# Kernel optimization log

Hardware: AMD Instinct MI355X
Metric: run time of the kernel (lower is better)

Reference implementation:

```python
import jax, jax.numpy as jnp
import numpy as np
from jax.scipy.special import logsumexp

K, V, D, R = 512, 50257, 768, 192
S_ITERS = 10
LAMBDA_MAHAL = 0.3
GAMMA_SINKHORN = 0.3


def setup_inputs() -> dict:
    key = jax.random.key(0)
    ks = jax.random.split(key, 6)
    word_embeds = jax.random.normal(ks[0], (V, D), dtype=jnp.float32)
    # warm-start anchors: mean word embed + small noise (as in torch init)
    anchors = jnp.broadcast_to(word_embeds.mean(axis=0, keepdims=True), (K, D)) \
        + jax.random.normal(ks[1], (K, D), dtype=jnp.float32) * 0.05
    return {
        "word_embeds": word_embeds,
        "concept_anchors": anchors,
        "M_U": jax.random.normal(ks[2], (D, R), dtype=jnp.float32) * 0.01,
        "log_eps": jnp.float32(-1.5),
        "log_scale": jnp.float32(0.0),
        "topic_bias": jnp.zeros((K, 1), dtype=jnp.float32),
        "word_proj_w": jnp.eye(D, dtype=jnp.float32),
    }


def _normalize(x, eps=1e-12):
    n = jnp.sqrt(jnp.sum(x * x, axis=-1, keepdims=True))
    return x / jnp.maximum(n, eps)


def _mahalanobis_cost(A, B, M_U):
    # M = I + U U^T  (low-rank update); C[k,v] = (a-b)^T M (a-b)
    M = jnp.eye(A.shape[-1], dtype=A.dtype) + M_U @ M_U.T
    MA = A @ M          # [K, D]
    MB = B @ M          # [V, D]
    AA = jnp.sum(MA * A, axis=-1, keepdims=True)       # [K, 1]
    BB = jnp.sum(MB * B, axis=-1, keepdims=True).T     # [1, V]
    AB = MA @ B.T                                      # [K, V]
    return jax.nn.relu(AA + BB - 2.0 * AB)


def _sinkhorn_log(log_K):
    def body(_, carry):
        log_u, log_v = carry
        log_u = -logsumexp(log_K + log_v, axis=1, keepdims=True)  # [K,1]
        log_v = -logsumexp(log_K + log_u, axis=0, keepdims=True)  # [1,V]
        return log_u, log_v
    log_u0 = jnp.zeros((log_K.shape[0], 1), log_K.dtype)
    log_v0 = jnp.zeros((1, log_K.shape[1]), log_K.dtype)
    log_u, log_v = jax.lax.fori_loop(0, S_ITERS, body, (log_u0, log_v0))
    return log_K + log_u + log_v


def reference(word_embeds, concept_anchors, M_U, log_eps, log_scale,
              topic_bias, word_proj_w):
    w = _normalize(word_embeds @ word_proj_w.T)     # [V, D]
    a = _normalize(concept_anchors)                 # [K, D]
    scale = jnp.minimum(jnp.exp(log_scale), 20.0)
    direct_logits = scale * (a @ w.T) + topic_bias  # [K, V]
    mahal = _mahalanobis_cost(a, w, M_U)            # [K, V]
    eps = jax.nn.softplus(log_eps) + 0.001
    log_P = _sinkhorn_log(-mahal / eps)             # [K, V]
    logits = direct_logits - LAMBDA_MAHAL * mahal + GAMMA_SINKHORN * log_P
    logits = jnp.clip(logits, -30.0, 30.0)
    return jax.nn.softmax(logits, axis=-1)
```

## Files before the change

### kernel.cpp

```cpp
#include <hip/hip_runtime.h>
#include <math.h>

#define KK 512
#define VV 50257
#define VP 50272
#define DD 768
#define RR 192

#define LAM 0.3f
#define GAM 0.3f
#define L2E 1.44269504088896340736f
#define ENC_NEG_INF 0x007FFFFFu

typedef __bf16 bf16x8 __attribute__((ext_vector_type(8)));
typedef _Float16 f16x8 __attribute__((ext_vector_type(8)));
typedef _Float16 f16x2 __attribute__((ext_vector_type(2)));
typedef unsigned short u16x8 __attribute__((ext_vector_type(8)));
typedef float f32x4 __attribute__((ext_vector_type(4)));

static __device__ __forceinline__ float get_eps(const float* p_log_eps) {
  return log1pf(expf(p_log_eps[0])) + 0.001f;
}

static __device__ __forceinline__ float fast_exp2(float x) {
  return __builtin_amdgcn_exp2f(x);
}

static __device__ __forceinline__ unsigned enc_f(float f) {
  unsigned u = __builtin_bit_cast(unsigned, f);
  return (u & 0x80000000u) ? ~u : (u | 0x80000000u);
}
static __device__ __forceinline__ float dec_f(unsigned e) {
  unsigned u = (e & 0x80000000u) ? (e ^ 0x80000000u) : ~e;
  return __builtin_bit_cast(float, u);
}

static __device__ __forceinline__ unsigned short f2bf(float x) {
  unsigned u = __builtin_bit_cast(unsigned, x);
  u += 0x7fffu + ((u >> 16) & 1u);
  return (unsigned short)(u >> 16);
}
static __device__ __forceinline__ float bf2f(unsigned short h) {
  unsigned u = ((unsigned)h) << 16;
  return __builtin_bit_cast(float, u);
}

static __device__ __forceinline__ void gload_lds16(const void* g, void* l) {
  __builtin_amdgcn_global_load_lds(
      (const __attribute__((address_space(1))) unsigned int*)g,
      (__attribute__((address_space(3))) unsigned int*)l, 16, 0, 0);
}

__global__ __launch_bounds__(256)
void prep(const float* __restrict__ U, float* __restrict__ lv2,
          unsigned* __restrict__ slots, const float* __restrict__ anchors,
          _Float16* __restrict__ Ut16, _Float16* __restrict__ a16) {
  int bid = blockIdx.x;
  int t = threadIdx.x;
  if (bid < 576) {
    int idx = bid * 256 + t;
    int r = idx / DD;
    int d = idx - r * DD;
    Ut16[idx] = (_Float16)U[(size_t)d * RR + r];
  } else if (bid < 773) {
    int i = (bid - 576) * 256 + t;
    if (i < 50264) lv2[i] = 0.f;
  } else if (bid == 773) {
    if (t < 24) slots[t] = (t == 0) ? 0x80000000u : ENC_NEG_INF;
    if (t == 24) slots[24] = 1u;
  } else {
    int r = bid - 774;
    const float* x = anchors + (size_t)r * DD;
    float v0 = x[t], v1 = x[t + 256], v2 = x[t + 512];
    __shared__ float red[256];
    red[t] = v0 * v0 + v1 * v1 + v2 * v2;
    __syncthreads();
    for (int off = 128; off > 0; off >>= 1) {
      if (t < off) red[t] += red[t + off];
      __syncthreads();
    }
    float inv = 1.0f / fmaxf(sqrtf(red[0]), 1e-12f);
    _Float16* y = a16 + (size_t)r * DD;
    y[t] = (_Float16)(v0 * inv);
    y[t + 256] = (_Float16)(v1 * inv);
    y[t + 512] = (_Float16)(v2 * inv);
  }
}

__global__ __launch_bounds__(256)
void check_eye(const float* __restrict__ Wp, unsigned* __restrict__ flag) {
  int i = blockIdx.x * 256 + threadIdx.x;
  if (i >= DD * DD) return;
  int r = i / DD;
  int c = i - r * DD;
  float expect = (r == c) ? 1.f : 0.f;
  if (Wp[i] != expect) atomicAnd(flag, 0u);
}

#define BM 128
#define BN 128
#define BK 32
#define LDKB 40
#define LDK 40

__global__ __launch_bounds__(256, 2)
void gemm_we_fallback(const float* __restrict__ A, const float* __restrict__ B,
                      _Float16* __restrict__ C, int M, int N, int Kd,
                      const unsigned* __restrict__ eyeflag) {
  if (*eyeflag) return;
  __shared__ unsigned short As[2][BM][LDKB];
  __shared__ unsigned short Bs[2][BN][LDKB];
  const int tid = threadIdx.x;
  const int bm = blockIdx.y * BM;
  const int bn = blockIdx.x * BN;
  const int srow = tid >> 1;
  const int skb = (tid & 1) << 4;
  const int wave = tid >> 6;
  const int lane = tid & 63;
  const int wm = (wave >> 1) << 6;
  const int wn = (wave & 1) << 6;
  const int lm = lane & 15;
  const int quad = lane >> 4;
  f32x4 acc[4][4];
#pragma unroll
  for (int i = 0; i < 4; ++i)
#pragma unroll
    for (int j = 0; j < 4; ++j) acc[i][j] = (f32x4){0.f, 0.f, 0.f, 0.f};
  const int ra = bm + srow;
  const int rb = bn + srow;
  for (int k0 = 0; k0 < Kd; k0 += BK) {
    float va[16], vb[16];
    if (ra < M) {
      const float4* p = (const float4*)(A + (size_t)ra * Kd + k0 + skb);
      ((float4*)va)[0] = p[0]; ((float4*)va)[1] = p[1];
      ((float4*)va)[2] = p[2]; ((float4*)va)[3] = p[3];
    } else {
#pragma unroll
      for (int q = 0; q < 16; ++q) va[q] = 0.f;
    }
    if (rb < N) {
      const float4* p = (const float4*)(B + (size_t)rb * Kd + k0 + skb);
      ((float4*)vb)[0] = p[0]; ((float4*)vb)[1] = p[1];
      ((float4*)vb)[2] = p[2]; ((float4*)vb)[3] = p[3];
    } else {
#pragma unroll
      for (int q = 0; q < 16; ++q) vb[q] = 0.f;
    }
    __syncthreads();
    {
      u16x8 h0, h1, l0, l1;
#pragma unroll
      for (int q = 0; q < 8; ++q) {
        unsigned short h = f2bf(va[q]);
        h0[q] = h; l0[q] = f2bf(va[q] - bf2f(h));
        h = f2bf(va[q + 8]);
        h1[q] = h; l1[q] = f2bf(va[q + 8] - bf2f(h));
      }
      *(u16x8*)&As[0][srow][skb] = h0; *(u16x8*)&As[0][srow][skb + 8] = h1;
      *(u16x8*)&As[1][srow][skb] = l0; *(u16x8*)&As[1][srow][skb + 8] = l1;
#pragma unroll
      for (int q = 0; q < 8; ++q) {
        unsigned short h = f2bf(vb[q]);
        h0[q] = h; l0[q] = f2bf(vb[q] - bf2f(h));
        h = f2bf(vb[q + 8]);
        h1[q] = h; l1[q] = f2bf(vb[q + 8] - bf2f(h));
      }
      *(u16x8*)&Bs[0][srow][skb] = h0; *(u16x8*)&Bs[0][srow][skb + 8] = h1;
      *(u16x8*)&Bs[1][srow][skb] = l0; *(u16x8*)&Bs[1][srow][skb + 8] = l1;
    }
    __syncthreads();
    bf16x8 Ah[4], Al[4], Bh[4], Bl[4];
#pragma unroll
    for (int i = 0; i < 4; ++i) {
      Ah[i] = *(const bf16x8*)&As[0][wm + i * 16 + lm][quad * 8];
      Al[i] = *(const bf16x8*)&As[1][wm + i * 16 + lm][quad * 8];
      Bh[i] = *(const bf16x8*)&Bs[0][wn + i * 16 + lm][quad * 8];
      Bl[i] = *(const bf16x8*)&Bs[1][wn + i * 16 + lm][quad * 8];
    }
#pragma unroll
    for (int i = 0; i < 4; ++i)
#pragma unroll
      for (int j = 0; j < 4; ++j) {
        acc[i][j] = __builtin_amdgcn_mfma_f32_16x16x32_bf16(Ah[i], Bh[j], acc[i][j], 0, 0, 0);
        acc[i][j] = __builtin_amdgcn_mfma_f32_16x16x32_bf16(Ah[i], Bl[j], acc[i][j], 0, 0, 0);
        acc[i][j] = __builtin_amdgcn_mfma_f32_16x16x32_bf16(Al[i], Bh[j], acc[i][j], 0, 0, 0);
      }
  }
#pragma unroll
  for (int i = 0; i < 4; ++i)
#pragma unroll
    for (int j = 0; j < 4; ++j) {
      int col = bn + wn + j * 16 + lm;
#pragma unroll
      for (int r = 0; r < 4; ++r) {
        int row = bm + wm + i * 16 + quad * 4 + r;
        if (row < M && col < N) C[(size_t)row * N + col] = (_Float16)acc[i][j][r];
      }
    }
}

__global__ __launch_bounds__(256)
void norm_w(const float* __restrict__ WE, _Float16* __restrict__ w16,
            const unsigned* __restrict__ eyeflag) {
  int r = blockIdx.x;
  int t = threadIdx.x;
  float v0, v1, v2;
  if (*eyeflag) {
    const float* x = WE + (size_t)r * DD;
    v0 = x[t]; v1 = x[t + 256]; v2 = x[t + 512];
  } else {
    const _Float16* x = w16 + (size_t)r * DD;
    v0 = (float)x[t]; v1 = (float)x[t + 256]; v2 = (float)x[t + 512];
  }
  __shared__ float red[256];
  red[t] = v0 * v0 + v1 * v1 + v2 * v2;
  __syncthreads();
  for (int off = 128; off > 0; off >>= 1) {
    if (t < off) red[t] += red[t + off];
    __syncthreads();
  }
  float inv = 1.0f / fmaxf(sqrtf(red[0]), 1e-12f);
  _Float16* y = w16 + (size_t)r * DD;
  y[t] = (_Float16)(v0 * inv);
  y[t + 256] = (_Float16)(v1 * inv);
  y[t + 512] = (_Float16)(v2 * inv);
}

template <int F16OUT>
__global__ __launch_bounds__(256, 2)
void gemm16(const _Float16* __restrict__ A, const _Float16* __restrict__ B,
            void* __restrict__ Cv, int M, int N, int Kd) {
  __shared__ _Float16 As[BM][LDK];
  __shared__ _Float16 Bs[BN][LDK];
  const int tid = threadIdx.x;
  const int bm = blockIdx.y * BM;
  const int bn = blockIdx.x * BN;
  const int srow = tid >> 1;
  const int skb = (tid & 1) << 4;
  const int wave = tid >> 6;
  const int lane = tid & 63;
  const int wm = (wave >> 1) << 6;
  const int wn = (wave & 1) << 6;
  const int lm = lane & 15;
  const int quad = lane >> 4;
  f32x4 acc[4][4];
#pragma unroll
  for (int i = 0; i < 4; ++i)
#pragma unroll
    for (int j = 0; j < 4; ++j) acc[i][j] = (f32x4){0.f, 0.f, 0.f, 0.f};
  const int ra = bm + srow;
  const int rb = bn + srow;
  for (int k0 = 0; k0 < Kd; k0 += BK) {
    f16x8 a0 = (f16x8)(_Float16)0, a1 = a0, b0 = a0, b1 = a0;
    if (ra < M) {
      const f16x8* p = (const f16x8*)(A + (size_t)ra * Kd + k0 + skb);
      a0 = p[0]; a1 = p[1];
    }
    if (rb < N) {
      const f16x8* p = (const f16x8*)(B + (size_t)rb * Kd + k0 + skb);
      b0 = p[0]; b1 = p[1];
    }
    __syncthreads();
    *(f16x8*)&As[srow][skb] = a0; *(f16x8*)&As[srow][skb + 8] = a1;
    *(f16x8*)&Bs[srow][skb] = b0; *(f16x8*)&Bs[srow][skb + 8] = b1;
    __syncthreads();
    f16x8 Af[4], Bf[4];
#pragma unroll
    for (int i = 0; i < 4; ++i) {
      Af[i] = *(const f16x8*)&As[wm + i * 16 + lm][quad * 8];
      Bf[i] = *(const f16x8*)&Bs[wn + i * 16 + lm][quad * 8];
    }
#pragma unroll
    for (int i = 0; i < 4; ++i)
#pragma unroll
      for (int j = 0; j < 4; ++j)
        acc[i][j] = __builtin_amdgcn_mfma_f32_16x16x32_f16(Af[i], Bf[j], acc[i][j], 0, 0, 0);
  }
#pragma unroll
  for (int i = 0; i < 4; ++i)
#pragma unroll
    for (int j = 0; j < 4; ++j) {
      int col = bn + wn + j * 16 + lm;
#pragma unroll
      for (int r = 0; r < 4; ++r) {
        int row = bm + wm + i * 16 + quad * 4 + r;
        if (row < M && col < N) {
          if (F16OUT)
            ((_Float16*)Cv)[(size_t)row * N + col] = (_Float16)acc[i][j][r];
          else
            ((float*)Cv)[(size_t)row * N + col] = acc[i][j][r];
        }
      }
    }
}

__global__ __launch_bounds__(256, 2)
void gemm_sp(const _Float16* __restrict__ Aw, const _Float16* __restrict__ Bw,
             const _Float16* __restrict__ Au, const _Float16* __restrict__ Bu,
             float* __restrict__ Sd, _Float16* __restrict__ mhq,
             const float* __restrict__ AAv, const float* __restrict__ BBv,
             const float* __restrict__ tbias,
             const float* __restrict__ p_log_scale,
             const float* __restrict__ p_log_eps, int M, int N) {
  __shared__ _Float16 As[BM][32];
  __shared__ _Float16 Bs[BN][32];
  const int tid = threadIdx.x;
  const int bm = blockIdx.x * BM;
  const int bn = blockIdx.y * BN;
  const int wave = tid >> 6;
  const int lane = tid & 63;
  const int wm = (wave >> 1) << 6;
  const int wn = (wave & 1) << 6;
  const int lm = lane & 15;
  const int quad = lane >> 4;

  const int c0 = wave * 2;
  const int r0 = c0 * 16 + (lane >> 2);
  const int r1 = r0 + 16;
  const int gp = lane & 3;
  const int gg0 = gp ^ ((r0 >> 1) & 3);
  const int gg1 = gp ^ ((r1 >> 1) & 3);
  _Float16* ldsA0 = &As[0][0] + c0 * 512;
  _Float16* ldsA1 = ldsA0 + 512;
  _Float16* ldsB0 = &Bs[0][0] + c0 * 512;
  _Float16* ldsB1 = ldsB0 + 512;

  f32x4 accP[4][4];
#pragma unroll
  for (int i = 0; i < 4; ++i)
#pragma unroll
    for (int j = 0; j < 4; ++j) accP[i][j] = (f32x4){0.f, 0.f, 0.f, 0.f};

  {
    const _Float16* pa0 = Au + (size_t)(bm + r0) * RR + gg0 * 8;
    const _Float16* pa1 = Au + (size_t)(bm + r1) * RR + gg1 * 8;
    const _Float16* pb0 = Bu + (size_t)(bn + r0) * RR + gg0 * 8;
    const _Float16* pb1 = Bu + (size_t)(bn + r1) * RR + gg1 * 8;
    for (int k0 = 0; k0 < RR; k0 += BK) {
      gload_lds16(pa0 + k0, ldsA0);
      gload_lds16(pa1 + k0, ldsA1);
      gload_lds16(pb0 + k0, ldsB0);
      gload_lds16(pb1 + k0, ldsB1);
      __syncthreads();
      f16x8 Af[4], Bf[4];
#pragma unroll
      for (int i = 0; i < 4; ++i) {
        int ra_ = wm + i * 16 + lm;
        int rb_ = wn + i * 16 + lm;
        Af[i] = *(const f16x8*)&As[ra_][(quad ^ ((ra_ >> 1) & 3)) * 8];
        Bf[i] = *(const f16x8*)&Bs[rb_][(quad ^ ((rb_ >> 1) & 3)) * 8];
      }
#pragma unroll
      for (int i = 0; i < 4; ++i)
#pragma unroll
        for (int j = 0; j < 4; ++j)
          accP[i][j] = __builtin_amdgcn_mfma_f32_16x16x32_f16(Af[i], Bf[j], accP[i][j], 0, 0, 0);
      __syncthreads();
    }
  }

  f32x4 accS[4][4];
#pragma unroll
  for (int i = 0; i < 4; ++i)
#pragma unroll
    for (int j = 0; j < 4; ++j) accS[i][j] = (f32x4){0.f, 0.f, 0.f, 0.f};
  {
    const _Float16* pa0 = Aw + (size_t)(bm + r0) * DD + gg0 * 8;
    const _Float16* pa1 = Aw + (size_t)(bm + r1) * DD + gg1 * 8;
    const _Float16* pb0 = Bw + (size_t)(bn + r0) * DD + gg0 * 8;
    const _Float16* pb1 = Bw + (size_t)(bn + r1) * DD + gg1 * 8;
    for (int k0 = 0; k0 < DD; k0 += BK) {
      gload_lds16(pa0 + k0, ldsA0);
      gload_lds16(pa1 + k0, ldsA1);
      gload_lds16(pb0 + k0, ldsB0);
      gload_lds16(pb1 + k0, ldsB1);
      __syncthreads();
      f16x8 Af[4], Bf[4];
#pragma unroll
      for (int i = 0; i < 4; ++i) {
        int ra_ = wm + i * 16 + lm;
        int rb_ = wn + i * 16 + lm;
        Af[i] = *(const f16x8*)&As[ra_][(quad ^ ((ra_ >> 1) & 3)) * 8];
        Bf[i] = *(const f16x8*)&Bs[rb_][(quad ^ ((rb_ >> 1) & 3)) * 8];
      }
#pragma unroll
      for (int i = 0; i < 4; ++i)
#pragma unroll
        for (int j = 0; j < 4; ++j)
          accS[i][j] = __builtin_amdgcn_mfma_f32_16x16x32_f16(Af[i], Bf[j], accS[i][j], 0, 0, 0);
      __syncthreads();
    }
  }

  float scale = fminf(expf(p_log_scale[0]), 20.f);
  float qs = L2E / get_eps(p_log_eps);
#pragma unroll
  for (int i = 0; i < 4; ++i)
#pragma unroll
    for (int j = 0; j < 4; ++j) {
      int col = bn + wn + j * 16 + lm;
      if (col >= N) continue;
      float BB = BBv[col];
#pragma unroll
      for (int r = 0; r < 4; ++r) {
        int row = bm + wm + i * 16 + quad * 4 + r;
        float S = accS[i][j][r];
        float mh = fmaxf(AAv[row] + BB - 2.f * (S + accP[i][j][r]), 0.f);
        Sd[(size_t)row * N + col] = fmaf(scale, S, tbias[row]);
        mhq[(size_t)row * VP + col] = (_Float16)(mh * qs);
      }
    }
}

__global__ __launch_bounds__(256, 2)
void gemm16_p(const _Float16* __restrict__ A, const _Float16* __restrict__ B,
              float* __restrict__ Sd, _Float16* __restrict__ mhq,
              const float* __restrict__ AAv, const float* __restrict__ BBv,
              const float* __restrict__ tbias,
              const float* __restrict__ p_log_scale,
              const float* __restrict__ p_log_eps, int M, int N, int Kd) {
  __shared__ _Float16 As[BM][LDK];
  __shared__ _Float16 Bs[BN][LDK];
  const int tid = threadIdx.x;
  const int bm = blockIdx.y * BM;
  const int bn = blockIdx.x * BN;
  const int srow = tid >> 1;
  const int skb = (tid & 1) << 4;
  const int wave = tid >> 6;
  const int lane = tid & 63;
  const int wm = (wave >> 1) << 6;
  const int wn = (wave & 1) << 6;
  const int lm = lane & 15;
  const int quad = lane >> 4;
  f32x4 acc[4][4];
#pragma unroll
  for (int i = 0; i < 4; ++i)
#pragma unroll
    for (int j = 0; j < 4; ++j) acc[i][j] = (f32x4){0.f, 0.f, 0.f, 0.f};
  const int ra = bm + srow;
  const int rb = bn + srow;
  for (int k0 = 0; k0 < Kd; k0 += BK) {
    f16x8 a0 = (f16x8)(_Float16)0, a1 = a0, b0 = a0, b1 = a0;
    if (ra < M) {
      const f16x8* p = (const f16x8*)(A + (size_t)ra * Kd + k0 + skb);
      a0 = p[0]; a1 = p[1];
    }
    if (rb < N) {
      const f16x8* p = (const f16x8*)(B + (size_t)rb * Kd + k0 + skb);
      b0 = p[0]; b1 = p[1];
    }
    __syncthreads();
    *(f16x8*)&As[srow][skb] = a0; *(f16x8*)&As[srow][skb + 8] = a1;
    *(f16x8*)&Bs[srow][skb] = b0; *(f16x8*)&Bs[srow][skb + 8] = b1;
    __syncthreads();
    f16x8 Af[4], Bf[4];
#pragma unroll
    for (int i = 0; i < 4; ++i) {
      Af[i] = *(const f16x8*)&As[wm + i * 16 + lm][quad * 8];
      Bf[i] = *(const f16x8*)&Bs[wn + i * 16 + lm][quad * 8];
    }
#pragma unroll
    for (int i = 0; i < 4; ++i)
#pragma unroll
      for (int j = 0; j < 4; ++j)
        acc[i][j] = __builtin_amdgcn_mfma_f32_16x16x32_f16(Af[i], Bf[j], acc[i][j], 0, 0, 0);
  }
  float scale = fminf(expf(p_log_scale[0]), 20.f);
  float qs = L2E / get_eps(p_log_eps);
#pragma unroll
  for (int i = 0; i < 4; ++i)
#pragma unroll
    for (int j = 0; j < 4; ++j) {
      int col = bn + wn + j * 16 + lm;
      if (col >= N) continue;
      float BB = BBv[col];
#pragma unroll
      for (int r = 0; r < 4; ++r) {
        int row = bm + wm + i * 16 + quad * 4 + r;
        size_t idx = (size_t)row * N + col;
        float S = Sd[idx];
        float mh = fmaxf(AAv[row] + BB - 2.f * (S + acc[i][j][r]), 0.f);
        Sd[idx] = fmaf(scale, S, tbias[row]);
        mhq[(size_t)row * VP + col] = (_Float16)(mh * qs);
      }
    }
}

__global__ __launch_bounds__(256)
void row_sumsq16(const _Float16* __restrict__ X, float* __restrict__ out, int cols) {
  int r = blockIdx.x;
  int t = threadIdx.x;
  float x = (t < cols) ? (float)X[(size_t)r * cols + t] : 0.f;
  __shared__ float red[256];
  red[t] = x * x;
  __syncthreads();
  for (int off = 128; off > 0; off >>= 1) {
    if (t < off) red[t] += red[t + off];
    __syncthreads();
  }
  if (t == 0) out[r] = 1.0f + red[0];
}

__global__ __launch_bounds__(1024)
void sink_row(const _Float16* __restrict__ mhq, const float* __restrict__ lv2,
              float* __restrict__ lu2,
              const unsigned* __restrict__ Mv_slot, unsigned* __restrict__ Mu_slot) {
  int k = blockIdx.x;
  int t = threadIdx.x;
  float Mv2 = dec_f(*Mv_slot);
  const _Float16* row = mhq + (size_t)k * VP;
  float s[8] = {0.f, 0.f, 0.f, 0.f, 0.f, 0.f, 0.f, 0.f};
#pragma unroll
  for (int j = 0; j < 6; ++j) {
    int v = j * 8192 + t * 8;
    f16x8 hv = *(const f16x8*)(row + v);
    float4 l0 = *(const float4*)(lv2 + v);
    float4 l1 = *(const float4*)(lv2 + v + 4);
    float lv[8] = {l0.x, l0.y, l0.z, l0.w, l1.x, l1.y, l1.z, l1.w};
#pragma unroll
    for (int i = 0; i < 8; ++i)
      s[i] += fast_exp2(lv[i] - Mv2 - (float)hv[i]);
  }
  {
    int v = 49152 + t;
    s[0] += fast_exp2(lv2[v] - Mv2 - (float)row[v]);
    v = 50176 + t;
    if (v < VV) s[1] += fast_exp2(lv2[v] - Mv2 - (float)row[v]);
  }
  float sum = ((s[0] + s[1]) + (s[2] + s[3])) + ((s[4] + s[5]) + (s[6] + s[7]));
  __shared__ float red[1024];
  red[t] = sum;
  __syncthreads();
  for (int off = 512; off > 0; off >>= 1) {
    if (t < off) red[t] += red[t + off];
    __syncthreads();
  }
  if (t == 0) {
    float lu = -(Mv2 + log2f(red[0]));
    lu2[k] = lu;
    atomicMax(Mu_slot, enc_f(lu));
  }
}

__global__ __launch_bounds__(256)
void sink_col(const _Float16* __restrict__ mhq, const float* __restrict__ lu2,
              float* __restrict__ lv2,
              const unsigned* __restrict__ Mu_slot, unsigned* __restrict__ Mv_next) {
  __shared__ float lu_s[KK];
  int t = threadIdx.x;
  for (int i = t; i < KK; i += 256) lu_s[i] = lu2[i];
  __syncthreads();
  float Mu2 = dec_f(*Mu_slot);
  int cp = blockIdx.x * 64 + (t & 63);
  int v0 = cp * 2;
  int kc = t >> 6;
  float sA = 0.f, sB = 0.f;
  if (v0 < VV) {
    const _Float16* base = mhq + v0;
#pragma unroll 4
    for (int k = kc * 128; k < kc * 128 + 128; ++k) {
      f16x2 hv = *(const f16x2*)(base + (size_t)k * VP);
      float lu = lu_s[k] - Mu2;
      sA += fast_exp2(lu - (float)hv[0]);
      sB += fast_exp2(lu - (float)hv[1]);
    }
  }
  __shared__ float pA[256], pB[256];
  __shared__ unsigned em[64];
  pA[t] = sA; pB[t] = sB;
  __syncthreads();
  if (t < 64) {
    unsigned e = ENC_NEG_INF;
    if (v0 < VV) {
      float a = (pA[t] + pA[t + 64]) + (pA[t + 128] + pA[t + 192]);
      float lv = -(Mu2 + log2f(a));
      lv2[v0] = lv;
      e = enc_f(lv);
      if (v0 + 1 < VV) {
        float b = (pB[t] + pB[t + 64]) + (pB[t + 128] + pB[t + 192]);
        float lv1 = -(Mu2 + log2f(b));
        lv2[v0 + 1] = lv1;
        unsigned e1 = enc_f(lv1);
        if (e1 > e) e = e1;
      }
    }
    em[t] = e;
  }
  __syncthreads();
  for (int off = 32; off > 0; off >>= 1) {
    if (t < off && em[t + off] > em[t]) em[t] = em[t + off];
    __syncthreads();
  }
  if (t == 0) atomicMax(Mv_next, em[0]);
}

__global__ __launch_bounds__(1024)
void final_sum(const float* __restrict__ direct, const _Float16* __restrict__ mhq,
               const float* __restrict__ lu2, const float* __restrict__ lv2,
               float* __restrict__ row_s, const float* __restrict__ p_log_eps) {
  int k = blockIdx.x;
  int t = threadIdx.x;
  float eps = get_eps(p_log_eps);
  float c2 = (LAM * eps + GAM) / L2E;
  float c3 = GAM / L2E;
  float base_lu = c3 * lu2[k];
  const float* drow = direct + (size_t)k * VV;
  const _Float16* mrow = mhq + (size_t)k * VP;
  float s[8] = {0.f, 0.f, 0.f, 0.f, 0.f, 0.f, 0.f, 0.f};
#pragma unroll
  for (int j = 0; j < 6; ++j) {
    int v = j * 8192 + t * 8;
    f16x8 hv = *(const f16x8*)(mrow + v);
    float4 d0 = *(const float4*)(drow + v);
    float4 d1 = *(const float4*)(drow + v + 4);
    float4 l0 = *(const float4*)(lv2 + v);
    float4 l1 = *(const float4*)(lv2 + v + 4);
    float dd[8] = {d0.x, d0.y, d0.z, d0.w, d1.x, d1.y, d1.z, d1.w};
    float lv[8] = {l0.x, l0.y, l0.z, l0.w, l1.x, l1.y, l1.z, l1.w};
#pragma unroll
    for (int i = 0; i < 8; ++i) {
      float x = fmaf(-c2, (float)hv[i], fmaf(c3, lv[i], dd[i] + base_lu));
      x = fminf(30.f, fmaxf(-30.f, x));
      s[i] += fast_exp2(fmaf(x, L2E, -30.f * L2E));
    }
  }
  {
    int v = 49152 + t;
    float x = fmaf(-c2, (float)mrow[v], fmaf(c3, lv2[v], drow[v] + base_lu));
    x = fminf(30.f, fmaxf(-30.f, x));
    s[0] += fast_exp2(fmaf(x, L2E, -30.f * L2E));
    v = 50176 + t;
    if (v < VV) {
      x = fmaf(-c2, (float)mrow[v], fmaf(c3, lv2[v], drow[v] + base_lu));
      x = fminf(30.f, fmaxf(-30.f, x));
      s[1] += fast_exp2(fmaf(x, L2E, -30.f * L2E));
    }
  }
  float sum = ((s[0] + s[1]) + (s[2] + s[3])) + ((s[4] + s[5]) + (s[6] + s[7]));
  __shared__ float red[1024];
  red[t] = sum;
  __syncthreads();
  for (int off = 512; off > 0; off >>= 1) {
    if (t < off) red[t] += red[t + off];
    __syncthreads();
  }
  if (t == 0) row_s[k] = red[0];
}

__global__ __launch_bounds__(256)
void final_write(float* __restrict__ out, const _Float16* __restrict__ mhq,
                 const float* __restrict__ lu2, const float* __restrict__ lv2,
                 const float* __restrict__ row_s, const float* __restrict__ p_log_eps) {
  int v = blockIdx.x * 256 + threadIdx.x;
  int k = blockIdx.y;
  if (v >= VV) return;
  float eps = get_eps(p_log_eps);
  float c2 = (LAM * eps + GAM) / L2E;
  float c3 = GAM / L2E;
  size_t idx = (size_t)k * VV + v;
  float x = fmaf(-c2, (float)mhq[(size_t)k * VP + v],
                 fmaf(c3, lv2[v], out[idx] + c3 * lu2[k]));
  x = fminf(30.f, fmaxf(-30.f, x));
  out[idx] = fast_exp2(fmaf(x, L2E, -30.f * L2E)) / row_s[k];
}

extern "C" void kernel_launch(void* const* d_in, const int* in_sizes, int n_in,
                              void* d_out, int out_size, void* d_ws, size_t ws_size,
                              hipStream_t stream) {
  (void)in_sizes; (void)n_in; (void)out_size;
  const float* WE        = (const float*)d_in[0];
  const float* anchors   = (const float*)d_in[1];
  const float* MU        = (const float*)d_in[2];
  const float* log_eps   = (const float*)d_in[3];
  const float* log_scale = (const float*)d_in[4];
  const float* tbias     = (const float*)d_in[5];
  const float* Wp        = (const float*)d_in[6];
  float* out = (float*)d_out;

  const size_t H_W16 = (size_t)VV * DD;
  const size_t H_MHQ = (size_t)KK * VP;
  const size_t H_WU  = (size_t)VV * RR;
  const size_t H_A16 = (size_t)KK * DD;
  const size_t H_AU  = (size_t)KK * RR;
  const size_t H_UT  = (size_t)RR * DD;
  const size_t FB_FLOATS = 102064 + 32;
  const size_t need_roomy =
      2 * (H_W16 + H_MHQ + H_WU + H_A16 + H_AU + H_UT) + 4 * FB_FLOATS;
  const bool roomy = ws_size >= need_roomy;

  _Float16* hb = (_Float16*)d_ws;
  _Float16* w16 = hb;
  size_t ho = H_W16;
  _Float16* mhq;
  if (roomy) { mhq = hb + ho; ho += H_MHQ; }
  else       { mhq = hb; }
  _Float16* wU16 = hb + ho; ho += H_WU;
  _Float16* a16  = hb + ho; ho += H_A16;
  _Float16* aU16 = hb + ho; ho += H_AU;
  _Float16* Ut16 = hb + ho; ho += H_UT;
  float* fb = (float*)(hb + ho);
  float* BBv   = fb;
  float* AAv   = fb + 50264;
  float* lu2   = fb + 50776;
  float* lv2   = fb + 51288;
  float* row_s = fb + 101552;
  unsigned* slots = (unsigned*)(fb + 102064);
  unsigned* Mv_slots = slots;
  unsigned* Mu_slots = slots + 12;
  unsigned* eye_flag = slots + 24;

  const int VB = (VV + 255) / 256;
  const int MB_V = (VV + BM - 1) / BM;

  prep<<<1286, 256, 0, stream>>>(MU, lv2, slots, anchors, Ut16, a16);
  check_eye<<<(DD * DD + 255) / 256, 256, 0, stream>>>(Wp, eye_flag);
  gemm_we_fallback<<<dim3(DD / BN, MB_V), 256, 0, stream>>>(WE, Wp, w16, VV, DD, DD, eye_flag);
  norm_w<<<VV, 256, 0, stream>>>(WE, w16, eye_flag);
  gemm16<1><<<dim3(2, MB_V), 256, 0, stream>>>(w16, Ut16, wU16, VV, RR, DD);
  gemm16<1><<<dim3(2, 4), 256, 0, stream>>>(a16, Ut16, aU16, KK, RR, DD);
  row_sumsq16<<<VV, 256, 0, stream>>>(wU16, BBv, RR);
  row_sumsq16<<<KK, 256, 0, stream>>>(aU16, AAv, RR);
  if (roomy) {
    gemm_sp<<<dim3(4, MB_V), 256, 0, stream>>>(a16, w16, aU16, wU16, out, mhq,
                                               AAv, BBv, tbias, log_scale,
                                               log_eps, KK, VV);
  } else {
    gemm16<0><<<dim3(MB_V, 4), 256, 0, stream>>>(a16, w16, out, KK, VV, DD);
    gemm16_p<<<dim3(MB_V, 4), 256, 0, stream>>>(aU16, wU16, out, mhq, AAv, BBv,
                                                tbias, log_scale, log_eps, KK, VV, RR);
  }
  for (int it = 0; it < 10; ++it) {
    sink_row<<<KK, 1024, 0, stream>>>(mhq, lv2, lu2, Mv_slots + it, Mu_slots + it);
    sink_col<<<MB_V, 256, 0, stream>>>(mhq, lu2, lv2, Mu_slots + it, Mv_slots + it + 1);
  }
  final_sum<<<KK, 1024, 0, stream>>>(out, mhq, lu2, lv2, row_s, log_eps);
  final_write<<<dim3(VB, KK), 256, 0, stream>>>(out, mhq, lu2, lv2, row_s, log_eps);
}
```

Measured before the change: 907.6 us.

## Double-buffer LDS tiles in fused cost GEMM to overlap global loads with MFMA

The gemm_sp kernel now keeps two LDS buffers for the A and B tiles and issues the next K-slice's global-to-LDS loads before computing on the current slice. It waits with explicit vmcnt counters and raw s_barrier instead of __syncthreads. The low-rank and full-dimension GEMM phases are merged into one 30-step staged pipeline. This aims to hide global memory latency behind the matrix instructions, at the cost of doubled LDS usage, which could lower occupancy, and hand-managed wait counts that must match the number of outstanding loads.

Measured after the change: 910.3 us. Within noise of the previous version (+0.3%).

```diff
diff --git a/kernel.cpp b/kernel.cpp
--- a/kernel.cpp
+++ b/kernel.cpp
@@ -302,8 +302,8 @@
              const float* __restrict__ tbias,
              const float* __restrict__ p_log_scale,
              const float* __restrict__ p_log_eps, int M, int N) {
-  __shared__ _Float16 As[BM][32];
-  __shared__ _Float16 Bs[BN][32];
+  __shared__ _Float16 As[2][BM][32];
+  __shared__ _Float16 Bs[2][BM][32];
   const int tid = threadIdx.x;
   const int bm = blockIdx.x * BM;
   const int bn = blockIdx.y * BN;
@@ -320,76 +320,91 @@
   const int gp = lane & 3;
   const int gg0 = gp ^ ((r0 >> 1) & 3);
   const int gg1 = gp ^ ((r1 >> 1) & 3);
-  _Float16* ldsA0 = &As[0][0] + c0 * 512;
-  _Float16* ldsA1 = ldsA0 + 512;
-  _Float16* ldsB0 = &Bs[0][0] + c0 * 512;
-  _Float16* ldsB1 = ldsB0 + 512;
-
-  f32x4 accP[4][4];
+
+  const _Float16* pAu0 = Au + (size_t)(bm + r0) * RR + gg0 * 8;
+  const _Float16* pAu1 = Au + (size_t)(bm + r1) * RR + gg1 * 8;
+  const _Float16* pBu0 = Bu + (size_t)(bn + r0) * RR + gg0 * 8;
+  const _Float16* pBu1 = Bu + (size_t)(bn + r1) * RR + gg1 * 8;
+  const _Float16* pAw0 = Aw + (size_t)(bm + r0) * DD + gg0 * 8;
+  const _Float16* pAw1 = Aw + (size_t)(bm + r1) * DD + gg1 * 8;
+  const _Float16* pBw0 = Bw + (size_t)(bn + r0) * DD + gg0 * 8;
+  const _Float16* pBw1 = Bw + (size_t)(bn + r1) * DD + gg1 * 8;
+
+  auto stage = [&](int t, int buf) {
+    _Float16* la = &As[buf][0][0] + c0 * 512;
+    _Float16* lb = &Bs[buf][0][0] + c0 * 512;
+    if (t < 6) {
+      int k0 = t * BK;
+      gload_lds16(pAu0 + k0, la);
+      gload_lds16(pAu1 + k0, la + 512);
+      gload_lds16(pBu0 + k0, lb);
+      gload_lds16(pBu1 + k0, lb + 512);
+    } else {
+      int k0 = (t - 6) * BK;
+      gload_lds16(pAw0 + k0, la);
+      gload_lds16(pAw1 + k0, la + 512);
+      gload_lds16(pBw0 + k0, lb);
+      gload_lds16(pBw1 + k0, lb + 512);
+    }
+  };
+
+  f32x4 accP[4][4], accS[4][4];
 #pragma unroll
   for (int i = 0; i < 4; ++i)
 #pragma unroll
-    for (int j = 0; j < 4; ++j) accP[i][j] = (f32x4){0.f, 0.f, 0.f, 0.f};
-
-  {
-    const _Float16* pa0 = Au + (size_t)(bm + r0) * RR + gg0 * 8;
-    const _Float16* pa1 = Au + (size_t)(bm + r1) * RR + gg1 * 8;
-    const _Float16* pb0 = Bu + (size_t)(bn + r0) * RR + gg0 * 8;
-    const _Float16* pb1 = Bu + (size_t)(bn + r1) * RR + gg1 * 8;
-    for (int k0 = 0; k0 < RR; k0 += BK) {
-      gload_lds16(pa0 + k0, ldsA0);
-      gload_lds16(pa1 + k0, ldsA1);
-      gload_lds16(pb0 + k0, ldsB0);
-      gload_lds16(pb1 + k0, ldsB1);
-      __syncthreads();
-      f16x8 Af[4], Bf[4];
-#pragma unroll
-      for (int i = 0; i < 4; ++i) {
-        int ra_ = wm + i * 16 + lm;
-        int rb_ = wn + i * 16 + lm;
-        Af[i] = *(const f16x8*)&As[ra_][(quad ^ ((ra_ >> 1) & 3)) * 8];
-        Bf[i] = *(const f16x8*)&Bs[rb_][(quad ^ ((rb_ >> 1) & 3)) * 8];
-      }
-#pragma unroll
-      for (int i = 0; i < 4; ++i)
-#pragma unroll
-        for (int j = 0; j < 4; ++j)
-          accP[i][j] = __builtin_amdgcn_mfma_f32_16x16x32_f16(Af[i], Bf[j], accP[i][j], 0, 0, 0);
-      __syncthreads();
-    }
-  }
-
-  f32x4 accS[4][4];
-#pragma unroll
-  for (int i = 0; i < 4; ++i)
-#pragma unroll
-    for (int j = 0; j < 4; ++j) accS[i][j] = (f32x4){0.f, 0.f, 0.f, 0.f};
-  {
-    const _Float16* pa0 = Aw + (size_t)(bm + r0) * DD + gg0 * 8;
-    const _Float16* pa1 = Aw + (size_t)(bm + r1) * DD + gg1 * 8;
-    const _Float16* pb0 = Bw + (size_t)(bn + r0) * DD + gg0 * 8;
-    const _Float16* pb1 = Bw + (size_t)(bn + r1) * DD + gg1 * 8;
-    for (int k0 = 0; k0 < DD; k0 += BK) {
-      gload_lds16(pa0 + k0, ldsA0);
-      gload_lds16(pa1 + k0, ldsA1);
-      gload_lds16(pb0 + k0, ldsB0);
-      gload_lds16(pb1 + k0, ldsB1);
-      __syncthreads();
-      f16x8 Af[4], Bf[4];
-#pragma unroll
-      for (int i = 0; i < 4; ++i) {
-        int ra_ = wm + i * 16 + lm;
-        int rb_ = wn + i * 16 + lm;
-        Af[i] = *(const f16x8*)&As[ra_][(quad ^ ((ra_ >> 1) & 3)) * 8];
-        Bf[i] = *(const f16x8*)&Bs[rb_][(quad ^ ((rb_ >> 1) & 3)) * 8];
-      }
-#pragma unroll
-      for (int i = 0; i < 4; ++i)
-#pragma unroll
-        for (int j = 0; j < 4; ++j)
-          accS[i][j] = __builtin_amdgcn_mfma_f32_16x16x32_f16(Af[i], Bf[j], accS[i][j], 0, 0, 0);
-      __syncthreads();
-    }
+    for (int j = 0; j < 4; ++j) {
+      accP[i][j] = (f32x4){0.f, 0.f, 0.f, 0.f};
+      accS[i][j] = (f32x4){0.f, 0.f, 0.f, 0.f};
+    }
+
+  stage(0, 0);
+  for (int t = 0; t < 6; ++t) {
+    const int cur = t & 1;
+    stage(t + 1, cur ^ 1);
+    asm volatile("s_waitcnt vmcnt(4)" ::: "memory");
+    __builtin_amdgcn_s_barrier();
+    asm volatile("" ::: "memory");
+    f16x8 Af[4], Bf[4];
+#pragma unroll
+    for (int i = 0; i < 4; ++i) {
+      int ra_ = wm + i * 16 + lm;
+      int rb_ = wn + i * 16 + lm;
+      Af[i] = *(const f16x8*)&As[cur][ra_][(quad ^ ((ra_ >> 1) & 3)) * 8];
+      Bf[i] = *(const f16x8*)&Bs[cur][rb_][(quad ^ ((rb_ >> 1) & 3)) * 8];
+    }
+#pragma unroll
+    for (int i = 0; i < 4; ++i)
+#pragma unroll
+      for (int j = 0; j < 4; ++j)
+        accP[i][j] = __builtin_amdgcn_mfma_f32_16x16x32_f16(Af[i], Bf[j], accP[i][j], 0, 0, 0);
+    asm volatile("" ::: "memory");
+    __builtin_amdgcn_s_barrier();
+  }
+  for (int t = 6; t < 30; ++t) {
+    const int cur = t & 1;
+    if (t < 29) {
+      stage(t + 1, cur ^ 1);
+      asm volatile("s_waitcnt vmcnt(4)" ::: "memory");
+    } else {
+      asm volatile("s_waitcnt vmcnt(0)" ::: "memory");
+    }
+    __builtin_amdgcn_s_barrier();
+    asm volatile("" ::: "memory");
+    f16x8 Af[4], Bf[4];
+#pragma unroll
+    for (int i = 0; i < 4; ++i) {
+      int ra_ = wm + i * 16 + lm;
+      int rb_ = wn + i * 16 + lm;
+      Af[i] = *(const f16x8*)&As[cur][ra_][(quad ^ ((ra_ >> 1) & 3)) * 8];
+      Bf[i] = *(const f16x8*)&Bs[cur][rb_][(quad ^ ((rb_ >> 1) & 3)) * 8];
+    }
+#pragma unroll
+    for (int i = 0; i < 4; ++i)
+#pragma unroll
+      for (int j = 0; j < 4; ++j)
+        accS[i][j] = __builtin_amdgcn_mfma_f32_16x16x32_f16(Af[i], Bf[j], accS[i][j], 0, 0, 0);
+    asm volatile("" ::: "memory");
+    __builtin_amdgcn_s_barrier();
   }
 
   float scale = fminf(expf(p_log_scale[0]), 20.f);
```
